# Performance work log

Measured on AMD Instinct MI355X. Metric: run time of the kernel, lower is better.

## Reference

```python
import jax, jax.numpy as jnp
import numpy as np

INPUT_SIZE = 512
HIDDEN = 1024
N_QP = 64
M_QP = 128
QP_ITER = 50
MIN_EIG = 0.01
N_P = N_QP * (N_QP + 1) // 2              # 2080
N_H = M_QP * N_QP                          # 8192
N_OUT = N_P + N_QP + N_H + M_QP            # 10464
BATCH = 1024


def setup_inputs() -> dict:
    key = jax.random.key(0)
    ks = jax.random.split(key, 4)
    s = lambda fan_in: np.float32(1.0 / np.sqrt(fan_in))
    return {
        "x": jax.random.normal(ks[0], (BATCH, INPUT_SIZE), jnp.float32),
        "W1": jax.random.normal(ks[1], (INPUT_SIZE, HIDDEN), jnp.float32) * s(INPUT_SIZE),
        "b1": jnp.zeros((HIDDEN,), jnp.float32),
        "W2": jax.random.normal(ks[2], (HIDDEN, HIDDEN), jnp.float32) * s(HIDDEN),
        "b2": jnp.zeros((HIDDEN,), jnp.float32),
        "W3": jax.random.normal(ks[3], (HIDDEN, N_OUT), jnp.float32) * s(HIDDEN),
        "b3": jnp.zeros((N_OUT,), jnp.float32),
    }


def _make_psd(p):
    # p: (bs, n(n+1)/2) packed row-major lower triangle of Cholesky factor L.
    # Diagonal entries (index i(i+1)/2 - 1) -> sqrt(min_eig) + softplus, so P = L L' is PSD.
    bs = p.shape[0]
    i = jnp.arange(1, N_QP + 1)
    diag_idx = i * (i + 1) // 2 - 1
    p = p.at[:, diag_idx].set(np.float32(np.sqrt(MIN_EIG)) + jax.nn.softplus(p[:, diag_idx]))
    r, c = jnp.tril_indices(N_QP)
    L = jnp.zeros((bs, N_QP, N_QP), p.dtype).at[:, r, c].set(p)
    return jnp.einsum('bik,bjk->bij', L, L)


def _forward(x, W1, b1, W2, b2, W3, b3):
    # MLP generating QP parameters (P, q, H, b)
    h = jax.nn.relu(x @ W1 + b1)
    h = jax.nn.relu(h @ W2 + b2)
    out = h @ W3 + b3                               # (bs, N_OUT)
    P_params = out[:, :N_P]
    q = out[:, N_P:N_P + N_QP]                      # (bs, n)
    H = out[:, N_P + N_QP:N_P + N_QP + N_H].reshape(-1, M_QP, N_QP)  # (bs, m, n)
    b = out[:, N_P + N_QP + N_H:]                   # (bs, m)
    P = _make_psd(P_params)                         # (bs, n, n)

    # Step sizes: tau = sigma = 0.9 / ||H||_2, spectral norm via 10 fixed power iterations
    v = jnp.ones((x.shape[0], N_QP), x.dtype) / np.float32(np.sqrt(N_QP))
    for _ in range(10):
        w = jnp.einsum('bmn,bm->bn', H, jnp.einsum('bmn,bn->bm', H, v))
        v = w / (jnp.linalg.norm(w, axis=1, keepdims=True) + 1e-12)
    sn = jnp.linalg.norm(jnp.einsum('bmn,bn->bm', H, v), axis=1) + 1e-6
    tau = (0.9 / sn)[:, None]                       # (bs, 1) primal step
    sig = tau                                       # dual step

    # Precompute (I + tau P)^{-1} once; fixed across PDHG iterations
    eye = jnp.eye(N_QP, dtype=x.dtype)
    Minv = jnp.linalg.inv(eye[None] + tau[:, :, None] * P)

    x0 = jnp.zeros((x.shape[0], N_QP), x.dtype)
    lam0 = jnp.zeros((x.shape[0], M_QP), x.dtype)

    def step(carry, _):
        xp, xbar, lam = carry
        lam = jax.nn.relu(lam - sig * (jnp.einsum('bmn,bn->bm', H, xbar) + b))
        xn = jnp.einsum('bnk,bk->bn', Minv, xp + tau * (jnp.einsum('bmn,bm->bn', H, lam) - q))
        return (xn, 2.0 * xn - xp, lam), None

    (xs, _, _), _ = jax.lax.scan(step, (x0, x0, lam0), None, length=QP_ITER)
    return xs  # (bs, n_qp): last primal iterate, matching solver(...)[1][:, -1, :]


def reference(x, W1, b1, W2, b2, W3, b3):
    return _forward(x, W1, b1, W2, b2, W3, b3)
```

## Files before the change

kernel.cpp:

```cpp
#include <hip/hip_runtime.h>
#include <cstdint>

typedef unsigned short u16;
typedef __attribute__((ext_vector_type(8))) short short8;
typedef __attribute__((ext_vector_type(4))) float floatx4;
typedef __attribute__((ext_vector_type(4))) float f4;

#define NQP   64
#define MQP   128
#define NP    2080
#define NHH   8192
#define NOUT  10464
#define NOUTP 10496

__device__ __forceinline__ float b2f(u16 u) {
  union { unsigned int i; float f; } v; v.i = ((unsigned int)u) << 16; return v.f;
}
__device__ __forceinline__ u16 f2b(float f) {
  union { float f; unsigned int i; } v; v.f = f;
  unsigned int r = v.i + 0x7fffu + ((v.i >> 16) & 1u);
  return (u16)(r >> 16);
}

__global__ __launch_bounds__(256) void detect_dtype(const u16* __restrict__ w,
                                                    int* __restrict__ flag) {
  __shared__ int cnt;
  if (threadIdx.x == 0) cnt = 0;
  __syncthreads();
  int c = 0;
  for (int i = threadIdx.x; i < 16384; i += 256) {
    const int e = (w[i] >> 7) & 0xFF;
    if (e >= 130 || e <= 90) ++c;
  }
  atomicAdd(&cnt, c);
  __syncthreads();
  if (threadIdx.x == 0) flag[0] = (cnt > 3000) ? 1 : 0;
}

__device__ __forceinline__ u16 load_elem_bf16(const void* p, size_t idx, int isf32) {
  return isf32 ? f2b(((const float*)p)[idx]) : ((const u16*)p)[idx];
}

__global__ __launch_bounds__(256) void convert_bf16(const void* __restrict__ in,
                                                    u16* __restrict__ out, int n,
                                                    const int* __restrict__ flag) {
  const int isf = flag[0];
  for (int i = blockIdx.x * 256 + threadIdx.x; i < n; i += gridDim.x * 256)
    out[i] = load_elem_bf16(in, i, isf);
}

__global__ __launch_bounds__(256) void conv_biases(const void* __restrict__ b1,
                                                   const void* __restrict__ b2,
                                                   const void* __restrict__ b3,
                                                   float* __restrict__ bf1,
                                                   float* __restrict__ bf2,
                                                   float* __restrict__ bf3,
                                                   const int* __restrict__ flag) {
  const int isf = flag[0];
  const int i = blockIdx.x * 256 + threadIdx.x;
  if (i < 1024) {
    bf1[i] = isf ? ((const float*)b1)[i] : b2f(((const u16*)b1)[i]);
  } else if (i < 2048) {
    const int j = i - 1024;
    bf2[j] = isf ? ((const float*)b2)[j] : b2f(((const u16*)b2)[j]);
  } else if (i < 2048 + NOUT) {
    const int j = i - 2048;
    bf3[j] = isf ? ((const float*)b3)[j] : b2f(((const u16*)b3)[j]);
  }
}

__global__ __launch_bounds__(256) void transpose_all(const void* __restrict__ W1,
                                                     const void* __restrict__ W2,
                                                     const void* __restrict__ W3,
                                                     u16* __restrict__ W1t,
                                                     u16* __restrict__ W2t,
                                                     u16* __restrict__ W3t,
                                                     const int* __restrict__ flag) {
  const int bx = blockIdx.x, by = blockIdx.y;
  const void* in; u16* out; int K, N, Npad, bxo;
  if (bx < 32)      { in = W1; out = W1t; K = 512;  N = 1024; Npad = 1024;  bxo = 0;
                      if (by >= 16) return; }
  else if (bx < 64) { in = W2; out = W2t; K = 1024; N = 1024; Npad = 1024;  bxo = 32; }
  else              { in = W3; out = W3t; K = 1024; N = NOUT; Npad = NOUTP; bxo = 64; }
  __shared__ u16 tile[32][33];
  const int isf = flag[0];
  const int n0 = (bx - bxo) * 32, k0 = by * 32;
  const int tx = threadIdx.x & 31, ty = threadIdx.x >> 5;
#pragma unroll
  for (int i = 0; i < 4; ++i) {
    const int k = k0 + ty + 8 * i, n = n0 + tx;
    tile[ty + 8 * i][tx] = (n < N) ? load_elem_bf16(in, (size_t)k * N + n, isf) : (u16)0;
  }
  __syncthreads();
#pragma unroll
  for (int i = 0; i < 4; ++i) {
    const int n = n0 + ty + 8 * i, k = k0 + tx;
    if (n < Npad) out[(size_t)n * K + k] = tile[tx][ty + 8 * i];
  }
}

__device__ __forceinline__ void gload_lds16(const u16* g, u16* l) {
  __builtin_amdgcn_global_load_lds((const __attribute__((address_space(1))) void*)g,
                                   (__attribute__((address_space(3))) void*)l, 16, 0, 0);
}

template <int EPI, bool HAS_LO>
__global__ __launch_bounds__(256) void gemm_bt(const u16* __restrict__ Ahi, const u16* __restrict__ Alo,
                                               const u16* __restrict__ Bt,  const float* __restrict__ bias,
                                               u16* __restrict__ Chi, u16* __restrict__ Clo,
                                               float* __restrict__ Cf,
                                               int M, int N, int K) {
  __shared__ __align__(16) u16 lA[128 * 32];
  __shared__ __align__(16) u16 lAlo[128 * 32];
  __shared__ __align__(16) u16 lB[128 * 32];
  const int tile_n = blockIdx.x * 128;
  const int tile_m = blockIdx.y * 128;
  const int lane = threadIdx.x & 63;
  const int wv   = threadIdx.x >> 6;
  const int wm = (wv & 1) * 64;
  const int wn = (wv >> 1) * 64;
  const int sr = lane >> 2;
  const int sk = (lane & 3) * 8;
  floatx4 acc[4][4] = {};

  for (int k0 = 0; k0 < K; k0 += 32) {
#pragma unroll
    for (int it = 0; it < 2; ++it) {
      const int slot = it * 4 + wv;
      const int r = slot * 16 + sr;
      gload_lds16(Ahi + (size_t)(tile_m + r) * K + k0 + sk, lA + slot * 512);
      if (HAS_LO)
        gload_lds16(Alo + (size_t)(tile_m + r) * K + k0 + sk, lAlo + slot * 512);
      gload_lds16(Bt + (size_t)(tile_n + r) * K + k0 + sk, lB + slot * 512);
    }
    __syncthreads();
    const int ro = lane & 15;
    const int qo = (lane >> 4) * 8;
    short8 af[4], bfr[4], al[4];
#pragma unroll
    for (int i = 0; i < 4; ++i) af[i] = *(const short8*)(lA + (wm + i * 16 + ro) * 32 + qo);
#pragma unroll
    for (int j = 0; j < 4; ++j) bfr[j] = *(const short8*)(lB + (wn + j * 16 + ro) * 32 + qo);
    if (HAS_LO) {
#pragma unroll
      for (int i = 0; i < 4; ++i) al[i] = *(const short8*)(lAlo + (wm + i * 16 + ro) * 32 + qo);
    }
#pragma unroll
    for (int i = 0; i < 4; ++i)
#pragma unroll
      for (int j = 0; j < 4; ++j) {
        acc[i][j] = __builtin_amdgcn_mfma_f32_16x16x32_bf16(af[i], bfr[j], acc[i][j], 0, 0, 0);
        if (HAS_LO)
          acc[i][j] = __builtin_amdgcn_mfma_f32_16x16x32_bf16(al[i], bfr[j], acc[i][j], 0, 0, 0);
      }
    __syncthreads();
  }

  const int colb = tile_n + wn + (lane & 15);
  const int rowb = tile_m + wm + (lane >> 4) * 4;
#pragma unroll
  for (int j = 0; j < 4; ++j) {
    const int col = colb + j * 16;
    const float bv = (col < N) ? bias[col] : 0.f;
#pragma unroll
    for (int i = 0; i < 4; ++i) {
#pragma unroll
      for (int v = 0; v < 4; ++v) {
        const int row = rowb + i * 16 + v;
        float val = acc[i][j][v] + bv;
        if (EPI == 0) {
          val = fmaxf(val, 0.f);
          const u16 hi = f2b(val);
          const float lo = val - b2f(hi);
          Chi[(size_t)row * N + col] = hi;
          Clo[(size_t)row * N + col] = f2b(lo);
        } else if (EPI == 2) {
          val = fmaxf(val, 0.f);
          Chi[(size_t)row * N + col] = f2b(val);
        } else {
          if (col < N) Cf[(size_t)row * N + col] = val;
        }
      }
    }
  }
}

template <int EPI, bool HAS_LO>
__global__ __launch_bounds__(256) void gemm_bt64(const u16* __restrict__ Ahi, const u16* __restrict__ Alo,
                                                 const u16* __restrict__ Bt,  const float* __restrict__ bias,
                                                 u16* __restrict__ Chi, u16* __restrict__ Clo,
                                                 int N, int K) {
  __shared__ __align__(16) u16 lA[64 * 32];
  __shared__ __align__(16) u16 lAlo[64 * 32];
  __shared__ __align__(16) u16 lB[64 * 32];
  const int tile_n = blockIdx.x * 64;
  const int tile_m = blockIdx.y * 64;
  const int lane = threadIdx.x & 63;
  const int wv   = threadIdx.x >> 6;
  const int wm = (wv & 1) * 32;
  const int wn = (wv >> 1) * 32;
  const int sr = lane >> 2;
  const int sk = (lane & 3) * 8;
  floatx4 acc[2][2] = {};

  for (int k0 = 0; k0 < K; k0 += 32) {
    {
      const int r = wv * 16 + sr;
      gload_lds16(Ahi + (size_t)(tile_m + r) * K + k0 + sk, lA + wv * 512);
      if (HAS_LO)
        gload_lds16(Alo + (size_t)(tile_m + r) * K + k0 + sk, lAlo + wv * 512);
      gload_lds16(Bt + (size_t)(tile_n + r) * K + k0 + sk, lB + wv * 512);
    }
    __syncthreads();
    const int ro = lane & 15;
    const int qo = (lane >> 4) * 8;
    short8 af[2], bfr[2], al[2];
#pragma unroll
    for (int i = 0; i < 2; ++i) af[i] = *(const short8*)(lA + (wm + i * 16 + ro) * 32 + qo);
#pragma unroll
    for (int j = 0; j < 2; ++j) bfr[j] = *(const short8*)(lB + (wn + j * 16 + ro) * 32 + qo);
    if (HAS_LO) {
#pragma unroll
      for (int i = 0; i < 2; ++i) al[i] = *(const short8*)(lAlo + (wm + i * 16 + ro) * 32 + qo);
    }
#pragma unroll
    for (int i = 0; i < 2; ++i)
#pragma unroll
      for (int j = 0; j < 2; ++j) {
        acc[i][j] = __builtin_amdgcn_mfma_f32_16x16x32_bf16(af[i], bfr[j], acc[i][j], 0, 0, 0);
        if (HAS_LO)
          acc[i][j] = __builtin_amdgcn_mfma_f32_16x16x32_bf16(al[i], bfr[j], acc[i][j], 0, 0, 0);
      }
    __syncthreads();
  }

  const int colb = tile_n + wn + (lane & 15);
  const int rowb = tile_m + wm + (lane >> 4) * 4;
#pragma unroll
  for (int j = 0; j < 2; ++j) {
    const int col = colb + j * 16;
    const float bv = bias[col];
#pragma unroll
    for (int i = 0; i < 2; ++i) {
#pragma unroll
      for (int v = 0; v < 4; ++v) {
        const int row = rowb + i * 16 + v;
        float val = acc[i][j][v] + bv;
        val = fmaxf(val, 0.f);
        const u16 hi = f2b(val);
        Chi[(size_t)row * N + col] = hi;
        if (EPI == 0) {
          const float lo = val - b2f(hi);
          Clo[(size_t)row * N + col] = f2b(lo);
        }
      }
    }
  }
}

__device__ __forceinline__ f4 ld4s(const float* p) { return *(const f4*)p; }
__device__ __forceinline__ void st4s(float* p, f4 v) { *(f4*)p = v; }
__device__ __forceinline__ float dot4(f4 a, f4 b) {
  return fmaf(a.x, b.x, fmaf(a.y, b.y, fmaf(a.z, b.z, a.w * b.w)));
}
__device__ __forceinline__ f4 shx4(f4 v, int m) {
  f4 r;
  r.x = __shfl_xor(v.x, m, 64); r.y = __shfl_xor(v.y, m, 64);
  r.z = __shfl_xor(v.z, m, 64); r.w = __shfl_xor(v.w, m, 64);
  return r;
}
__device__ __forceinline__ int hQ(int m, int g) {
  return (m << 6) + (((g ^ (m & 15))) << 2);
}

__global__ __launch_bounds__(256, 4) void qp_solve(const float* __restrict__ outbuf,
                                                   void* __restrict__ xs,
                                                   const int* __restrict__ flag) {
  __shared__ __align__(16) float H_s[8192];
  __shared__ __align__(16) float lam_s[128];
  __shared__ __align__(16) float b_s[128];
  __shared__ __align__(16) float part_s[4][64];
  __shared__ __align__(16) float rhs_s[64];
  __shared__ __align__(16) float xb_s[64];
  __shared__ __align__(16) float xp_s[64];
  __shared__ __align__(16) float q_s[64];
  __shared__ __align__(16) float buf2[2][64];
  __shared__ float tau_sh;

  const int t = threadIdx.x;
  const int w = t >> 6, l = t & 63;
  const int am = 32 * w + (l >> 1), as = l & 1;
  const int bg = l & 15, bc = l >> 4;
  const int ci = 16 * w + (l >> 2), cc = l & 3;
  const int isf = flag[0];
  const float* ob = outbuf + (size_t)blockIdx.x * NOUT;

  float* Ld = H_s;
  float* ps = H_s + 4352;
  for (int e = t; e < 4352; e += 256) Ld[e] = 0.f;
  for (int e = t; e < NP; e += 256) ps[e] = ob[e];
  if (t < 64) q_s[t] = ob[NP + t];
  if (t >= 128 && t < 256) b_s[t - 128] = ob[NP + NQP + NHH + (t - 128)];
  __syncthreads();
  if (t < 64) {
    const int i = t + 1;
    const int d = i * (i + 1) / 2 - 1;
    const float xv = ps[d];
    ps[d] = 0.1f + (fmaxf(xv, 0.f) + log1pf(expf(-fabsf(xv))));
  }
  __syncthreads();
  for (int e = t; e < NP; e += 256) {
    int i = (int)((sqrtf(8.f * (float)e + 1.f) - 1.f) * 0.5f);
    while ((i + 1) * (i + 2) / 2 <= e) ++i;
    while (i * (i + 1) / 2 > e) --i;
    const int j = e - i * (i + 1) / 2;
    Ld[i * 68 + j] = ps[e];
  }
  __syncthreads();

  float M[16];
#pragma unroll
  for (int jj = 0; jj < 16; ++jj) M[jj] = 0.f;
#pragma unroll
  for (int h = 0; h < 2; ++h) {
    f4 Lr[8];
#pragma unroll
    for (int g = 0; g < 8; ++g) Lr[g] = ld4s(&Ld[ci * 68 + (h * 8 + g) * 4]);
#pragma unroll
    for (int jj = 0; jj < 16; ++jj) {
      const int j = 16 * cc + jj;
      float s = 0.f;
#pragma unroll
      for (int g = 0; g < 8; ++g) s += dot4(Lr[g], ld4s(&Ld[j * 68 + (h * 8 + g) * 4]));
      M[jj] += s;
    }
  }
  __syncthreads();

  for (int e = t; e < NHH; e += 256) {
    const int m = e >> 6, n = e & 63;
    H_s[hQ(m, n >> 2) + (n & 3)] = ob[NP + NQP + e];
  }
  if (t < 64) xb_s[t] = 0.125f;
  __syncthreads();

  for (int pi = 0; pi < 10; ++pi) {
    {
      float s = 0.f;
#pragma unroll
      for (int k = 0; k < 8; ++k) {
        const int g = 8 * as + k;
        s += dot4(ld4s(&H_s[hQ(am, g)]), ld4s(&xb_s[4 * g]));
      }
      s += __shfl_xor(s, 1, 64);
      if (as == 0) lam_s[am] = s;
    }
    __syncthreads();
    {
      f4 u = {0.f, 0.f, 0.f, 0.f};
#pragma unroll
      for (int k = 0; k < 8; ++k) {
        const int m = 32 * w + 8 * bc + k;
        u += ld4s(&H_s[hQ(m, bg)]) * lam_s[m];
      }
      u += shx4(u, 16); u += shx4(u, 32);
      if (l < 16) st4s(&part_s[w][4 * bg], u);
    }
    __syncthreads();
    if (t < 64) {
      const float u = part_s[0][t] + part_s[1][t] + part_s[2][t] + part_s[3][t];
      float ss = u * u;
#pragma unroll
      for (int o = 1; o <= 32; o <<= 1) ss += __shfl_xor(ss, o, 64);
      xb_s[t] = u / (sqrtf(ss) + 1e-12f);
    }
    __syncthreads();
  }
  {
    float s = 0.f;
#pragma unroll
    for (int k = 0; k < 8; ++k) {
      const int g = 8 * as + k;
      s += dot4(ld4s(&H_s[hQ(am, g)]), ld4s(&xb_s[4 * g]));
    }
    s += __shfl_xor(s, 1, 64);
    if (as == 0) lam_s[am] = s;
  }
  __syncthreads();
  if (t < 64) {
    const float a = lam_s[t], bb = lam_s[t + 64];
    float ss = a * a + bb * bb;
#pragma unroll
    for (int o = 1; o <= 32; o <<= 1) ss += __shfl_xor(ss, o, 64);
    if (t == 0) tau_sh = 0.9f / (sqrtf(ss) + 1e-6f);
  }
  __syncthreads();
  const float tau = tau_sh;

#pragma unroll
  for (int jj = 0; jj < 16; ++jj)
    M[jj] = tau * M[jj] + ((16 * cc + jj == ci) ? 1.0f : 0.0f);

  if (ci == 0) {
#pragma unroll
    for (int jj = 0; jj < 16; ++jj) buf2[0][16 * cc + jj] = M[jj];
  }
  __syncthreads();
#pragma unroll
  for (int k = 0; k < 64; ++k) {
    const int kb = k & 1;
    const int kc = k >> 4;
    const float d = 1.0f / buf2[kb][k];
    f4 rv[4];
#pragma unroll
    for (int u = 0; u < 4; ++u) rv[u] = ld4s(&buf2[kb][16 * cc + 4 * u]);
    const float f = __shfl(M[k & 15], (l & 60) | kc, 64);
    if (ci == k) {
#pragma unroll
      for (int jj = 0; jj < 16; ++jj) M[jj] = rv[jj >> 2][jj & 3] * d;
      if (cc == kc) M[k & 15] = d;
    } else {
#pragma unroll
      for (int jj = 0; jj < 16; ++jj)
        M[jj] = fmaf(-f, rv[jj >> 2][jj & 3] * d, M[jj]);
      if (cc == kc) M[k & 15] = -f * d;
    }
    if (k < 63 && ci == k + 1) {
#pragma unroll
      for (int jj = 0; jj < 16; ++jj) buf2[1 - kb][16 * cc + jj] = M[jj];
    }
    __syncthreads();
  }

  float c0;
  {
    float acc = 0.f;
#pragma unroll
    for (int u = 0; u < 4; ++u) {
      const f4 qv = ld4s(&q_s[16 * cc + 4 * u]);
      acc = fmaf(M[4 * u + 0], qv.x, acc);
      acc = fmaf(M[4 * u + 1], qv.y, acc);
      acc = fmaf(M[4 * u + 2], qv.z, acc);
      acc = fmaf(M[4 * u + 3], qv.w, acc);
    }
    acc += __shfl_xor(acc, 1, 64);
    acc += __shfl_xor(acc, 2, 64);
    c0 = tau * acc;
  }

  if (t < 64) { xb_s[t] = 0.f; xp_s[t] = 0.f; }
  float lam = 0.f, xpr = 0.f;
  const float br = b_s[am];
  __syncthreads();

  for (int it = 0; it < 50; ++it) {
    {
      float s = 0.f;
#pragma unroll
      for (int k = 0; k < 8; ++k) {
        const int g = 8 * as + k;
        s += dot4(ld4s(&H_s[hQ(am, g)]), ld4s(&xb_s[4 * g]));
      }
      s += __shfl_xor(s, 1, 64);
      lam = fmaxf(lam - tau * (s + br), 0.f);
      if (as == 0) lam_s[am] = lam;
    }
    __syncthreads();
    {
      f4 u = {0.f, 0.f, 0.f, 0.f};
#pragma unroll
      for (int k = 0; k < 8; ++k) {
        const int m = 32 * w + 8 * bc + k;
        u += ld4s(&H_s[hQ(m, bg)]) * lam_s[m];
      }
      u += shx4(u, 16); u += shx4(u, 32);
      if (l < 16) st4s(&part_s[w][4 * bg], u);
    }
    __syncthreads();
    if (t < 64) {
      const float uu = part_s[0][t] + part_s[1][t] + part_s[2][t] + part_s[3][t];
      rhs_s[t] = xp_s[t] + tau * uu;
    }
    __syncthreads();
    {
      float acc = 0.f;
#pragma unroll
      for (int u = 0; u < 4; ++u) {
        const f4 rv = ld4s(&rhs_s[16 * cc + 4 * u]);
        acc = fmaf(M[4 * u + 0], rv.x, acc);
        acc = fmaf(M[4 * u + 1], rv.y, acc);
        acc = fmaf(M[4 * u + 2], rv.z, acc);
        acc = fmaf(M[4 * u + 3], rv.w, acc);
      }
      acc += __shfl_xor(acc, 1, 64);
      acc += __shfl_xor(acc, 2, 64);
      if (cc == 0) {
        const float xn = acc - c0;
        xp_s[ci] = xn;
        xb_s[ci] = 2.f * xn - xpr;
        xpr = xn;
      }
    }
    __syncthreads();
  }

  if (cc == 0) {
    const size_t oi = (size_t)blockIdx.x * NQP + ci;
    if (isf) ((float*)xs)[oi] = xpr;
    else     ((u16*)xs)[oi]   = f2b(xpr);
  }
}

extern "C" void kernel_launch(void* const* d_in, const int* in_sizes, int n_in,
                              void* d_out, int out_size, void* d_ws, size_t ws_size,
                              hipStream_t stream) {
  const void* x  = d_in[0];
  const void* W1 = d_in[1];
  const void* b1 = d_in[2];
  const void* W2 = d_in[3];
  const void* b2 = d_in[4];
  const void* W3 = d_in[5];
  const void* b3 = d_in[6];

  char* ws = (char*)d_ws;
  size_t off = 0;
  auto take = [&](size_t bytes) -> char* {
    char* r = ws + off;
    off += (bytes + 255) & ~(size_t)255;
    return r;
  };
  int*   flag = (int*)take(256);
  float* bf1  = (float*)take(1024 * 4);
  float* bf2  = (float*)take(1024 * 4);
  float* bf3  = (float*)take((size_t)NOUT * 4);
  u16*   W3t  = (u16*)take((size_t)NOUTP * 1024 * 2);
  u16*   h2hi = (u16*)take(1024ull * 1024 * 2);
  char*  region = take(1024ull * NOUT * 4);
  float* outf = (float*)region;
  u16* xb   = (u16*)(region + 0);
  u16* W1t  = (u16*)(region + (1u << 20));
  u16* W2t  = (u16*)(region + (2u << 20));
  u16* h1hi = (u16*)(region + (4u << 20));
  u16* h1lo = (u16*)(region + (6u << 20));
  (void)ws_size; (void)in_sizes; (void)n_in; (void)out_size;

  detect_dtype<<<dim3(1), 256, 0, stream>>>((const u16*)W1, flag);

  convert_bf16<<<dim3(512), 256, 0, stream>>>(x, xb, 1024 * 512, flag);
  conv_biases<<<dim3(49), 256, 0, stream>>>(b1, b2, b3, bf1, bf2, bf3, flag);
  transpose_all<<<dim3(392, 32), 256, 0, stream>>>(W1, W2, W3, W1t, W2t, W3t, flag);

  gemm_bt64<0, false><<<dim3(16, 16), 256, 0, stream>>>(xb, nullptr, W1t, bf1,
                                                        h1hi, h1lo, 1024, 512);
  gemm_bt64<2, true><<<dim3(16, 16), 256, 0, stream>>>(h1hi, h1lo, W2t, bf2,
                                                       h2hi, nullptr, 1024, 1024);
  gemm_bt<1, false><<<dim3(NOUTP / 128, 8), 256, 0, stream>>>(h2hi, nullptr, W3t, bf3,
                                                              nullptr, nullptr, outf, 1024, NOUT, 1024);
  qp_solve<<<dim3(1024), 256, 0, stream>>>(outf, d_out, flag);
}
```

Measured before the change: 466.6 us.

## Solve each QP with a single wavefront using register-resident state and readlane broadcasts

Replaces the 256-thread per-batch QP solver with a 64-thread, one-wavefront kernel. All vectors (x, lambda, rhs, q, b) live in registers and are broadcast with readlane instead of shared-memory exchanges, which removes every __syncthreads in the power iteration, the Gauss-Jordan inversion and the 50 PDHG steps. Each lane now holds a full 64-entry row of the inverse, so register pressure and the serial work per lane both grow. Occupancy is limited by the 32KB of LDS per block.

```diff
diff --git a/kernel.cpp b/kernel.cpp
--- a/kernel.cpp
+++ b/kernel.cpp
@@ -259,253 +259,209 @@
 }
 
 __device__ __forceinline__ f4 ld4s(const float* p) { return *(const f4*)p; }
-__device__ __forceinline__ void st4s(float* p, f4 v) { *(f4*)p = v; }
 __device__ __forceinline__ float dot4(f4 a, f4 b) {
   return fmaf(a.x, b.x, fmaf(a.y, b.y, fmaf(a.z, b.z, a.w * b.w)));
 }
-__device__ __forceinline__ f4 shx4(f4 v, int m) {
-  f4 r;
-  r.x = __shfl_xor(v.x, m, 64); r.y = __shfl_xor(v.y, m, 64);
-  r.z = __shfl_xor(v.z, m, 64); r.w = __shfl_xor(v.w, m, 64);
-  return r;
+__device__ __forceinline__ float rdlane(float v, int lane) {
+  return __int_as_float(__builtin_amdgcn_readlane(__float_as_int(v), lane));
 }
 __device__ __forceinline__ int hQ(int m, int g) {
   return (m << 6) + (((g ^ (m & 15))) << 2);
 }
 
-__global__ __launch_bounds__(256, 4) void qp_solve(const float* __restrict__ outbuf,
-                                                   void* __restrict__ xs,
-                                                   const int* __restrict__ flag) {
+__global__ __launch_bounds__(64, 1) void qp_wave(const float* __restrict__ outbuf,
+                                                 void* __restrict__ xs,
+                                                 const int* __restrict__ flag) {
   __shared__ __align__(16) float H_s[8192];
-  __shared__ __align__(16) float lam_s[128];
-  __shared__ __align__(16) float b_s[128];
-  __shared__ __align__(16) float part_s[4][64];
-  __shared__ __align__(16) float rhs_s[64];
-  __shared__ __align__(16) float xb_s[64];
-  __shared__ __align__(16) float xp_s[64];
-  __shared__ __align__(16) float q_s[64];
-  __shared__ __align__(16) float buf2[2][64];
-  __shared__ float tau_sh;
-
-  const int t = threadIdx.x;
-  const int w = t >> 6, l = t & 63;
-  const int am = 32 * w + (l >> 1), as = l & 1;
-  const int bg = l & 15, bc = l >> 4;
-  const int ci = 16 * w + (l >> 2), cc = l & 3;
+  const int l = threadIdx.x;
   const int isf = flag[0];
   const float* ob = outbuf + (size_t)blockIdx.x * NOUT;
 
   float* Ld = H_s;
-  float* ps = H_s + 4352;
-  for (int e = t; e < 4352; e += 256) Ld[e] = 0.f;
-  for (int e = t; e < NP; e += 256) ps[e] = ob[e];
-  if (t < 64) q_s[t] = ob[NP + t];
-  if (t >= 128 && t < 256) b_s[t - 128] = ob[NP + NQP + NHH + (t - 128)];
-  __syncthreads();
-  if (t < 64) {
-    const int i = t + 1;
-    const int d = i * (i + 1) / 2 - 1;
-    const float xv = ps[d];
-    ps[d] = 0.1f + (fmaxf(xv, 0.f) + log1pf(expf(-fabsf(xv))));
-  }
-  __syncthreads();
-  for (int e = t; e < NP; e += 256) {
+  for (int e = l; e < 4352; e += 64) Ld[e] = 0.f;
+  __syncthreads();
+  for (int e = l; e < NP; e += 64) {
     int i = (int)((sqrtf(8.f * (float)e + 1.f) - 1.f) * 0.5f);
     while ((i + 1) * (i + 2) / 2 <= e) ++i;
     while (i * (i + 1) / 2 > e) --i;
     const int j = e - i * (i + 1) / 2;
-    Ld[i * 68 + j] = ps[e];
-  }
-  __syncthreads();
-
-  float M[16];
-#pragma unroll
-  for (int jj = 0; jj < 16; ++jj) M[jj] = 0.f;
-#pragma unroll
-  for (int h = 0; h < 2; ++h) {
-    f4 Lr[8];
-#pragma unroll
-    for (int g = 0; g < 8; ++g) Lr[g] = ld4s(&Ld[ci * 68 + (h * 8 + g) * 4]);
-#pragma unroll
-    for (int jj = 0; jj < 16; ++jj) {
-      const int j = 16 * cc + jj;
-      float s = 0.f;
-#pragma unroll
-      for (int g = 0; g < 8; ++g) s += dot4(Lr[g], ld4s(&Ld[j * 68 + (h * 8 + g) * 4]));
-      M[jj] += s;
-    }
-  }
-  __syncthreads();
-
-  for (int e = t; e < NHH; e += 256) {
+    Ld[i * 68 + j] = ob[e];
+  }
+  __syncthreads();
+  {
+    const float xv = Ld[l * 68 + l];
+    Ld[l * 68 + l] = 0.1f + (fmaxf(xv, 0.f) + log1pf(expf(-fabsf(xv))));
+  }
+  __syncthreads();
+
+  const float qreg = ob[NP + l];
+  const float br0  = ob[NP + NQP + NHH + l];
+  const float br1  = ob[NP + NQP + NHH + 64 + l];
+
+  float M[64];
+  {
+    f4 Lr[16];
+#pragma unroll
+    for (int g = 0; g < 16; ++g) Lr[g] = ld4s(&Ld[l * 68 + 4 * g]);
+#pragma unroll
+    for (int j = 0; j < 64; ++j) {
+      float sa = 0.f, sb = 0.f;
+#pragma unroll
+      for (int g = 0; g < 16; g += 2) {
+        sa += dot4(Lr[g],     ld4s(&Ld[j * 68 + 4 * g]));
+        sb += dot4(Lr[g + 1], ld4s(&Ld[j * 68 + 4 * g + 4]));
+      }
+      M[j] = sa + sb;
+    }
+  }
+  __syncthreads();
+
+  for (int e = l; e < NHH; e += 64) {
     const int m = e >> 6, n = e & 63;
     H_s[hQ(m, n >> 2) + (n & 3)] = ob[NP + NQP + e];
   }
-  if (t < 64) xb_s[t] = 0.125f;
-  __syncthreads();
-
-  for (int pi = 0; pi < 10; ++pi) {
-    {
-      float s = 0.f;
-#pragma unroll
-      for (int k = 0; k < 8; ++k) {
-        const int g = 8 * as + k;
-        s += dot4(ld4s(&H_s[hQ(am, g)]), ld4s(&xb_s[4 * g]));
-      }
-      s += __shfl_xor(s, 1, 64);
-      if (as == 0) lam_s[am] = s;
-    }
-    __syncthreads();
-    {
-      f4 u = {0.f, 0.f, 0.f, 0.f};
-#pragma unroll
-      for (int k = 0; k < 8; ++k) {
-        const int m = 32 * w + 8 * bc + k;
-        u += ld4s(&H_s[hQ(m, bg)]) * lam_s[m];
-      }
-      u += shx4(u, 16); u += shx4(u, 32);
-      if (l < 16) st4s(&part_s[w][4 * bg], u);
-    }
-    __syncthreads();
-    if (t < 64) {
-      const float u = part_s[0][t] + part_s[1][t] + part_s[2][t] + part_s[3][t];
-      float ss = u * u;
-#pragma unroll
-      for (int o = 1; o <= 32; o <<= 1) ss += __shfl_xor(ss, o, 64);
-      xb_s[t] = u / (sqrtf(ss) + 1e-12f);
-    }
-    __syncthreads();
-  }
+  __syncthreads();
+
+  int ha[16];
+#pragma unroll
+  for (int g = 0; g < 16; ++g) ha[g] = hQ(l, g);
+  int ca[16];
+#pragma unroll
+  for (int p = 0; p < 16; ++p) ca[p] = (((l >> 2) ^ p) << 2) + (l & 3);
+
+  float v = 0.125f;
+  float s0 = 0.f, s1 = 0.f;
+  for (int pi = 0; pi < 11; ++pi) {
+    float a0 = 0.f, a1 = 0.f, b0 = 0.f, b1 = 0.f;
+#pragma unroll
+    for (int g = 0; g < 16; g += 2) {
+      const f4 h0 = ld4s(&H_s[ha[g]]);
+      const f4 h2 = ld4s(&H_s[ha[g + 1]]);
+      const f4 h1 = ld4s(&H_s[ha[g] + 4096]);
+      const f4 h3 = ld4s(&H_s[ha[g + 1] + 4096]);
+      const float x0 = rdlane(v, 4 * g + 0), x1 = rdlane(v, 4 * g + 1);
+      const float x2 = rdlane(v, 4 * g + 2), x3 = rdlane(v, 4 * g + 3);
+      const float x4 = rdlane(v, 4 * g + 4), x5 = rdlane(v, 4 * g + 5);
+      const float x6 = rdlane(v, 4 * g + 6), x7 = rdlane(v, 4 * g + 7);
+      a0 = fmaf(h0.x, x0, fmaf(h0.y, x1, fmaf(h0.z, x2, fmaf(h0.w, x3, a0))));
+      b0 = fmaf(h2.x, x4, fmaf(h2.y, x5, fmaf(h2.z, x6, fmaf(h2.w, x7, b0))));
+      a1 = fmaf(h1.x, x0, fmaf(h1.y, x1, fmaf(h1.z, x2, fmaf(h1.w, x3, a1))));
+      b1 = fmaf(h3.x, x4, fmaf(h3.y, x5, fmaf(h3.z, x6, fmaf(h3.w, x7, b1))));
+    }
+    s0 = a0 + b0;
+    s1 = a1 + b1;
+    if (pi == 10) break;
+    float u0 = 0.f, u1 = 0.f, u2 = 0.f, u3 = 0.f;
+#pragma unroll
+    for (int m = 0; m < 64; m += 4) {
+      u0 = fmaf(H_s[ca[(m + 0) & 15] + (m + 0) * 64], rdlane(s0, m + 0), u0);
+      u1 = fmaf(H_s[ca[(m + 1) & 15] + (m + 1) * 64], rdlane(s0, m + 1), u1);
+      u2 = fmaf(H_s[ca[(m + 2) & 15] + (m + 2) * 64], rdlane(s0, m + 2), u2);
+      u3 = fmaf(H_s[ca[(m + 3) & 15] + (m + 3) * 64], rdlane(s0, m + 3), u3);
+    }
+#pragma unroll
+    for (int m = 0; m < 64; m += 4) {
+      u0 = fmaf(H_s[ca[(m + 0) & 15] + (m + 64) * 64], rdlane(s1, m + 0), u0);
+      u1 = fmaf(H_s[ca[(m + 1) & 15] + (m + 65) * 64], rdlane(s1, m + 1), u1);
+      u2 = fmaf(H_s[ca[(m + 2) & 15] + (m + 66) * 64], rdlane(s1, m + 2), u2);
+      u3 = fmaf(H_s[ca[(m + 3) & 15] + (m + 67) * 64], rdlane(s1, m + 3), u3);
+    }
+    const float u = (u0 + u1) + (u2 + u3);
+    float ss = u * u;
+#pragma unroll
+    for (int o = 1; o <= 32; o <<= 1) ss += __shfl_xor(ss, o, 64);
+    v = u / (sqrtf(ss) + 1e-12f);
+  }
+  float tau;
   {
-    float s = 0.f;
-#pragma unroll
-    for (int k = 0; k < 8; ++k) {
-      const int g = 8 * as + k;
-      s += dot4(ld4s(&H_s[hQ(am, g)]), ld4s(&xb_s[4 * g]));
-    }
-    s += __shfl_xor(s, 1, 64);
-    if (as == 0) lam_s[am] = s;
-  }
-  __syncthreads();
-  if (t < 64) {
-    const float a = lam_s[t], bb = lam_s[t + 64];
-    float ss = a * a + bb * bb;
+    float ss = s0 * s0 + s1 * s1;
 #pragma unroll
     for (int o = 1; o <= 32; o <<= 1) ss += __shfl_xor(ss, o, 64);
-    if (t == 0) tau_sh = 0.9f / (sqrtf(ss) + 1e-6f);
-  }
-  __syncthreads();
-  const float tau = tau_sh;
-
-#pragma unroll
-  for (int jj = 0; jj < 16; ++jj)
-    M[jj] = tau * M[jj] + ((16 * cc + jj == ci) ? 1.0f : 0.0f);
-
-  if (ci == 0) {
-#pragma unroll
-    for (int jj = 0; jj < 16; ++jj) buf2[0][16 * cc + jj] = M[jj];
-  }
-  __syncthreads();
+    tau = 0.9f / (sqrtf(ss) + 1e-6f);
+  }
+
+#pragma unroll
+  for (int j = 0; j < 64; ++j)
+    M[j] = tau * M[j] + ((j == l) ? 1.0f : 0.0f);
+
 #pragma unroll
   for (int k = 0; k < 64; ++k) {
-    const int kb = k & 1;
-    const int kc = k >> 4;
-    const float d = 1.0f / buf2[kb][k];
-    f4 rv[4];
-#pragma unroll
-    for (int u = 0; u < 4; ++u) rv[u] = ld4s(&buf2[kb][16 * cc + 4 * u]);
-    const float f = __shfl(M[k & 15], (l & 60) | kc, 64);
-    if (ci == k) {
-#pragma unroll
-      for (int jj = 0; jj < 16; ++jj) M[jj] = rv[jj >> 2][jj & 3] * d;
-      if (cc == kc) M[k & 15] = d;
-    } else {
-#pragma unroll
-      for (int jj = 0; jj < 16; ++jj)
-        M[jj] = fmaf(-f, rv[jj >> 2][jj & 3] * d, M[jj]);
-      if (cc == kc) M[k & 15] = -f * d;
-    }
-    if (k < 63 && ci == k + 1) {
-#pragma unroll
-      for (int jj = 0; jj < 16; ++jj) buf2[1 - kb][16 * cc + jj] = M[jj];
-    }
-    __syncthreads();
+    const float d  = 1.0f / rdlane(M[k], k);
+    const float fd = M[k] * d;
+    const bool piv = (l == k);
+#pragma unroll
+    for (int j = 0; j < 64; ++j) {
+      if (j == k) continue;
+      const float pr = rdlane(M[j], k);
+      M[j] = piv ? (pr * d) : fmaf(-fd, pr, M[j]);
+    }
+    M[k] = piv ? d : -fd;
   }
 
   float c0;
   {
-    float acc = 0.f;
-#pragma unroll
-    for (int u = 0; u < 4; ++u) {
-      const f4 qv = ld4s(&q_s[16 * cc + 4 * u]);
-      acc = fmaf(M[4 * u + 0], qv.x, acc);
-      acc = fmaf(M[4 * u + 1], qv.y, acc);
-      acc = fmaf(M[4 * u + 2], qv.z, acc);
-      acc = fmaf(M[4 * u + 3], qv.w, acc);
-    }
-    acc += __shfl_xor(acc, 1, 64);
-    acc += __shfl_xor(acc, 2, 64);
-    c0 = tau * acc;
-  }
-
-  if (t < 64) { xb_s[t] = 0.f; xp_s[t] = 0.f; }
-  float lam = 0.f, xpr = 0.f;
-  const float br = b_s[am];
-  __syncthreads();
-
+    float c0a = 0.f, c0b = 0.f, c0c = 0.f, c0d = 0.f;
+#pragma unroll
+    for (int j = 0; j < 64; j += 4) {
+      c0a = fmaf(M[j + 0], rdlane(qreg, j + 0), c0a);
+      c0b = fmaf(M[j + 1], rdlane(qreg, j + 1), c0b);
+      c0c = fmaf(M[j + 2], rdlane(qreg, j + 2), c0c);
+      c0d = fmaf(M[j + 3], rdlane(qreg, j + 3), c0d);
+    }
+    c0 = tau * ((c0a + c0b) + (c0c + c0d));
+  }
+
+  float xb = 0.f, xp = 0.f, xpr = 0.f, lam0 = 0.f, lam1 = 0.f;
   for (int it = 0; it < 50; ++it) {
-    {
-      float s = 0.f;
-#pragma unroll
-      for (int k = 0; k < 8; ++k) {
-        const int g = 8 * as + k;
-        s += dot4(ld4s(&H_s[hQ(am, g)]), ld4s(&xb_s[4 * g]));
-      }
-      s += __shfl_xor(s, 1, 64);
-      lam = fmaxf(lam - tau * (s + br), 0.f);
-      if (as == 0) lam_s[am] = lam;
-    }
-    __syncthreads();
-    {
-      f4 u = {0.f, 0.f, 0.f, 0.f};
-#pragma unroll
-      for (int k = 0; k < 8; ++k) {
-        const int m = 32 * w + 8 * bc + k;
-        u += ld4s(&H_s[hQ(m, bg)]) * lam_s[m];
-      }
-      u += shx4(u, 16); u += shx4(u, 32);
-      if (l < 16) st4s(&part_s[w][4 * bg], u);
-    }
-    __syncthreads();
-    if (t < 64) {
-      const float uu = part_s[0][t] + part_s[1][t] + part_s[2][t] + part_s[3][t];
-      rhs_s[t] = xp_s[t] + tau * uu;
-    }
-    __syncthreads();
-    {
-      float acc = 0.f;
-#pragma unroll
-      for (int u = 0; u < 4; ++u) {
-        const f4 rv = ld4s(&rhs_s[16 * cc + 4 * u]);
-        acc = fmaf(M[4 * u + 0], rv.x, acc);
-        acc = fmaf(M[4 * u + 1], rv.y, acc);
-        acc = fmaf(M[4 * u + 2], rv.z, acc);
-        acc = fmaf(M[4 * u + 3], rv.w, acc);
-      }
-      acc += __shfl_xor(acc, 1, 64);
-      acc += __shfl_xor(acc, 2, 64);
-      if (cc == 0) {
-        const float xn = acc - c0;
-        xp_s[ci] = xn;
-        xb_s[ci] = 2.f * xn - xpr;
-        xpr = xn;
-      }
-    }
-    __syncthreads();
-  }
-
-  if (cc == 0) {
-    const size_t oi = (size_t)blockIdx.x * NQP + ci;
+    float a0 = 0.f, a1 = 0.f, b0 = 0.f, b1 = 0.f;
+#pragma unroll
+    for (int g = 0; g < 16; g += 2) {
+      const f4 h0 = ld4s(&H_s[ha[g]]);
+      const f4 h2 = ld4s(&H_s[ha[g + 1]]);
+      const f4 h1 = ld4s(&H_s[ha[g] + 4096]);
+      const f4 h3 = ld4s(&H_s[ha[g + 1] + 4096]);
+      const float x0 = rdlane(xb, 4 * g + 0), x1 = rdlane(xb, 4 * g + 1);
+      const float x2 = rdlane(xb, 4 * g + 2), x3 = rdlane(xb, 4 * g + 3);
+      const float x4 = rdlane(xb, 4 * g + 4), x5 = rdlane(xb, 4 * g + 5);
+      const float x6 = rdlane(xb, 4 * g + 6), x7 = rdlane(xb, 4 * g + 7);
+      a0 = fmaf(h0.x, x0, fmaf(h0.y, x1, fmaf(h0.z, x2, fmaf(h0.w, x3, a0))));
+      b0 = fmaf(h2.x, x4, fmaf(h2.y, x5, fmaf(h2.z, x6, fmaf(h2.w, x7, b0))));
+      a1 = fmaf(h1.x, x0, fmaf(h1.y, x1, fmaf(h1.z, x2, fmaf(h1.w, x3, a1))));
+      b1 = fmaf(h3.x, x4, fmaf(h3.y, x5, fmaf(h3.z, x6, fmaf(h3.w, x7, b1))));
+    }
+    lam0 = fmaxf(lam0 - tau * ((a0 + b0) + br0), 0.f);
+    lam1 = fmaxf(lam1 - tau * ((a1 + b1) + br1), 0.f);
+    float u0 = 0.f, u1 = 0.f, u2 = 0.f, u3 = 0.f;
+#pragma unroll
+    for (int m = 0; m < 64; m += 4) {
+      u0 = fmaf(H_s[ca[(m + 0) & 15] + (m + 0) * 64], rdlane(lam0, m + 0), u0);
+      u1 = fmaf(H_s[ca[(m + 1) & 15] + (m + 1) * 64], rdlane(lam0, m + 1), u1);
+      u2 = fmaf(H_s[ca[(m + 2) & 15] + (m + 2) * 64], rdlane(lam0, m + 2), u2);
+      u3 = fmaf(H_s[ca[(m + 3) & 15] + (m + 3) * 64], rdlane(lam0, m + 3), u3);
+    }
+#pragma unroll
+    for (int m = 0; m < 64; m += 4) {
+      u0 = fmaf(H_s[ca[(m + 0) & 15] + (m + 64) * 64], rdlane(lam1, m + 0), u0);
+      u1 = fmaf(H_s[ca[(m + 1) & 15] + (m + 65) * 64], rdlane(lam1, m + 1), u1);
+      u2 = fmaf(H_s[ca[(m + 2) & 15] + (m + 66) * 64], rdlane(lam1, m + 2), u2);
+      u3 = fmaf(H_s[ca[(m + 3) & 15] + (m + 67) * 64], rdlane(lam1, m + 3), u3);
+    }
+    const float u = (u0 + u1) + (u2 + u3);
+    const float rhs = xp + tau * u;
+    float xa = 0.f, xbq = 0.f, xc = 0.f, xd = 0.f;
+#pragma unroll
+    for (int j = 0; j < 64; j += 4) {
+      xa  = fmaf(M[j + 0], rdlane(rhs, j + 0), xa);
+      xbq = fmaf(M[j + 1], rdlane(rhs, j + 1), xbq);
+      xc  = fmaf(M[j + 2], rdlane(rhs, j + 2), xc);
+      xd  = fmaf(M[j + 3], rdlane(rhs, j + 3), xd);
+    }
+    const float xn = ((xa + xbq) + (xc + xd)) - c0;
+    xp = xn; xb = 2.f * xn - xpr; xpr = xn;
+  }
+
+  {
+    const size_t oi = (size_t)blockIdx.x * NQP + l;
     if (isf) ((float*)xs)[oi] = xpr;
     else     ((u16*)xs)[oi]   = f2b(xpr);
   }
@@ -556,5 +512,5 @@
                                                        h2hi, nullptr, 1024, 1024);
   gemm_bt<1, false><<<dim3(NOUTP / 128, 8), 256, 0, stream>>>(h2hi, nullptr, W3t, bf3,
                                                               nullptr, nullptr, outf, 1024, NOUT, 1024);
-  qp_solve<<<dim3(1024), 256, 0, stream>>>(outf, d_out, flag);
-}
+  qp_wave<<<dim3(1024), 64, 0, stream>>>(outf, d_out, flag);
+}
```

Result: slower. 620.8 us (+33.0%).
